# Optimization experiments

Hardware: AMD Instinct MI355X
Metric: run time of the kernel (lower is better)

## Reference

```python
import jax, jax.numpy as jnp
import numpy as np
from jax import lax

N = 8192
TARGET_COMPONENTS = 1.0
TARGET_CYCLES = 0.0
WEIGHT = 1.0
THRESH_SHIFT = 2.0


def setup_inputs() -> dict:
    key = jax.random.key(0)
    x = jax.random.normal(key, (N, N), dtype=jnp.float32)
    # symmetrize so directed DFS traversal == undirected connectivity,
    # then shift so adj > 0 is sparse (realistic learned graph structure)
    adj = (x + x.T) * 0.5 - THRESH_SHIFT
    return {"adj": adj}


def _count_components(adj):
    """Connected components via min-label propagation (parallel equivalent
    of the serial DFS in the torch module for a symmetric adjacency)."""
    n = adj.shape[0]
    pos = adj > 0  # [n, n] bool edge mask
    labels0 = jnp.arange(n, dtype=jnp.int32)

    def body(state):
        labels, _ = state
        # min label among neighbors (n = sentinel for non-edges)
        neigh_min = jnp.min(jnp.where(pos, labels[None, :], jnp.int32(n)), axis=1)
        new_labels = jnp.minimum(labels, neigh_min)
        return new_labels, jnp.any(new_labels != labels)

    labels, _ = lax.while_loop(lambda s: s[1], body,
                               (labels0, jnp.array(True)))
    # exactly one node per component keeps its own (minimal) index
    return jnp.sum((labels == labels0).astype(jnp.int32))


def reference(adj):
    n = adj.shape[0]
    n_comp = _count_components(adj).astype(jnp.float32)
    n_edges = (jnp.sum((adj > 0).astype(jnp.int32)) // 2).astype(jnp.float32)
    betti_1 = n_edges - jnp.float32(n) + n_comp           # Betti-1 estimate
    n_cycles = jnp.maximum(jnp.float32(0.0), betti_1)
    component_loss = (n_comp - TARGET_COMPONENTS) ** 2
    cycle_loss = (n_cycles - TARGET_CYCLES) ** 2
    return WEIGHT * (component_loss + cycle_loss)
```

## Files before the change

### kernel.cpp

```cpp
#include <hip/hip_runtime.h>


#define NN 8192
#define SCAN_LDS_CAP 2048

__global__ __launch_bounds__(64) void init_kernel(int* counters) {
    if (threadIdx.x < 2) counters[threadIdx.x] = 0;
}

__global__ __launch_bounds__(256) void scan_kernel(const float* __restrict__ adj,
                                                   int* __restrict__ counters,
                                                   unsigned int* __restrict__ ebuf,
                                                   int cap) {
    __shared__ int lds_n;
    __shared__ int lds_base;
    __shared__ unsigned int lds_e[SCAN_LDS_CAP];
    if (threadIdx.x == 0) lds_n = 0;
    __syncthreads();

    int b = blockIdx.x;
    int c1 = 0;
    #pragma unroll
    for (int half = 0; half < 2; ++half) {
        int r = half ? (NN - 1 - b) : b;
        const float4* rowp = (const float4*)(adj + (size_t)r * NN);
        int nf4 = (r + 4) >> 2;
        for (int g = threadIdx.x; g < nf4; g += 256) {
            float4 v = rowp[g];
            int j0 = g << 2;
            float vv[4] = {v.x, v.y, v.z, v.w};
            #pragma unroll
            for (int c = 0; c < 4; ++c) {
                int j = j0 + c;
                bool pos = vv[c] > 0.0f;
                if (pos && j < r) {
                    int k = atomicAdd(&lds_n, 1);
                    unsigned int e = ((unsigned)r << 13) | (unsigned)j;
                    if (k < SCAN_LDS_CAP) lds_e[k] = e;
                    else {
                        int gk = atomicAdd(counters, 1);
                        if (gk < cap) ebuf[gk] = e;
                    }
                }
                c1 += (pos && j == r) ? 1 : 0;
            }
        }
    }
    #pragma unroll
    for (int off = 32; off > 0; off >>= 1) c1 += __shfl_down(c1, off, 64);
    if ((threadIdx.x & 63) == 0 && c1) atomicAdd(counters + 1, c1);

    __syncthreads();
    int n = lds_n < SCAN_LDS_CAP ? lds_n : SCAN_LDS_CAP;
    if (threadIdx.x == 0) lds_base = atomicAdd(counters, n);
    __syncthreads();
    int base = lds_base;
    for (int k = threadIdx.x; k < n; k += 256) {
        int idx = base + k;
        if (idx < cap) ebuf[idx] = lds_e[k];
    }
}

__device__ __forceinline__ int find_lds(volatile int* par, int x) {
    int p = par[x];
    while (p != x) {
        int gp = par[p];
        if (gp == p) return p;
        par[x] = gp;
        x = gp;
        p = par[x];
    }
    return x;
}

__device__ __forceinline__ void unite_lds(int* par_raw, volatile int* par,
                                          int a, int b) {
    int ra = find_lds(par, a);
    int rb = find_lds(par, b);
    while (ra != rb) {
        int hi = ra > rb ? ra : rb;
        int lo = ra ^ rb ^ hi;
        int prev = atomicCAS(&par_raw[hi], hi, lo);
        if (prev == hi) return;
        ra = find_lds(par, prev);
        rb = find_lds(par, lo);
    }
}

__global__ __launch_bounds__(1024) void union_final_kernel(
        const unsigned int* __restrict__ ebuf,
        const int* __restrict__ counters,
        int cap, float* __restrict__ out) {
    __shared__ int par[NN];
    __shared__ int wsum[16];
    volatile int* vpar = par;
    int tid = threadIdx.x;
    for (int i = tid; i < NN; i += 1024) par[i] = i;
    __syncthreads();

    int total_lower = counters[0];
    int m = total_lower < cap ? total_lower : cap;

    const int CH = 16384;
    for (int base = 0; base < m; base += CH) {
        int hi = base + CH < m ? base + CH : m;
        for (int i = base + tid; i < hi; i += 1024) {
            unsigned int e = ebuf[i];
            unite_lds(par, vpar, (int)(e >> 13), (int)(e & (NN - 1)));
        }
        __syncthreads();
        for (int i = tid; i < NN; i += 1024) par[i] = find_lds(vpar, i);
        __syncthreads();
    }

    int cnt = 0;
    for (int i = tid; i < NN; i += 1024) cnt += (par[i] == i) ? 1 : 0;
    #pragma unroll
    for (int off = 32; off > 0; off >>= 1) cnt += __shfl_down(cnt, off, 64);
    if ((tid & 63) == 0) wsum[tid >> 6] = cnt;
    __syncthreads();
    if (tid == 0) {
        int roots = 0;
        #pragma unroll
        for (int w = 0; w < 16; ++w) roots += wsum[w];
        long long total = 2LL * (long long)total_lower + (long long)counters[1];
        long long n_edges_i = total >> 1;
        double n_comp = (double)roots;
        double comp_loss = (n_comp - 1.0) * (n_comp - 1.0);
        double betti = (double)n_edges_i - (double)NN + n_comp;
        double cyc = betti > 0.0 ? betti : 0.0;
        out[0] = (float)(comp_loss + cyc * cyc);
    }
}

extern "C" void kernel_launch(void* const* d_in, const int* in_sizes, int n_in,
                              void* d_out, int out_size, void* d_ws, size_t ws_size,
                              hipStream_t stream) {
    const float* adj = (const float*)d_in[0];
    int* ws = (int*)d_ws;
    int* counters = ws;
    unsigned int* ebuf = (unsigned int*)(ws + 2);
    long long cap_ll = (long long)(ws_size / 4) - 2;
    int cap = cap_ll > 0x7fffffff ? 0x7fffffff : (cap_ll < 0 ? 0 : (int)cap_ll);
    float* out = (float*)d_out;

    init_kernel<<<1, 64, 0, stream>>>(counters);
    scan_kernel<<<NN / 2, 256, 0, stream>>>(adj, counters, ebuf, cap);
    union_final_kernel<<<1, 1024, 0, stream>>>(ebuf, counters, cap, out);
}
```

Measured before the change: 436.9 us.

## Replace union-find with iterative min-label hooking and unroll scan row loads

The single-block component kernel drops the lock-free union-find and instead runs repeated passes over the edge list. Each pass hooks labels with atomicMin, then does one pointer-jumping step and loops until nothing changes. The scan kernel now issues four independent float4 loads per thread before processing them, to expose more memory-level parallelism. The label propagation may need many full passes over all ~78K edges in one block, which could cost more than the union-find did.

```diff
diff --git a/kernel.cpp b/kernel.cpp
--- a/kernel.cpp
+++ b/kernel.cpp
@@ -20,13 +20,14 @@
 
     int b = blockIdx.x;
     int c1 = 0;
+
     #pragma unroll
     for (int half = 0; half < 2; ++half) {
         int r = half ? (NN - 1 - b) : b;
         const float4* rowp = (const float4*)(adj + (size_t)r * NN);
         int nf4 = (r + 4) >> 2;
-        for (int g = threadIdx.x; g < nf4; g += 256) {
-            float4 v = rowp[g];
+
+        auto process = [&](float4 v, int g) {
             int j0 = g << 2;
             float vv[4] = {v.x, v.y, v.z, v.w};
             #pragma unroll
@@ -44,8 +45,22 @@
                 }
                 c1 += (pos && j == r) ? 1 : 0;
             }
+        };
+
+        int g = threadIdx.x;
+        for (; g + 768 < nf4; g += 1024) {
+            float4 v0 = rowp[g];
+            float4 v1 = rowp[g + 256];
+            float4 v2 = rowp[g + 512];
+            float4 v3 = rowp[g + 768];
+            process(v0, g);
+            process(v1, g + 256);
+            process(v2, g + 512);
+            process(v3, g + 768);
         }
+        for (; g < nf4; g += 256) process(rowp[g], g);
     }
+
     #pragma unroll
     for (int off = 32; off > 0; off >>= 1) c1 += __shfl_down(c1, off, 64);
     if ((threadIdx.x & 63) == 0 && c1) atomicAdd(counters + 1, c1);
@@ -61,60 +76,53 @@
     }
 }
 
-__device__ __forceinline__ int find_lds(volatile int* par, int x) {
-    int p = par[x];
-    while (p != x) {
-        int gp = par[p];
-        if (gp == p) return p;
-        par[x] = gp;
-        x = gp;
-        p = par[x];
-    }
-    return x;
-}
-
-__device__ __forceinline__ void unite_lds(int* par_raw, volatile int* par,
-                                          int a, int b) {
-    int ra = find_lds(par, a);
-    int rb = find_lds(par, b);
-    while (ra != rb) {
-        int hi = ra > rb ? ra : rb;
-        int lo = ra ^ rb ^ hi;
-        int prev = atomicCAS(&par_raw[hi], hi, lo);
-        if (prev == hi) return;
-        ra = find_lds(par, prev);
-        rb = find_lds(par, lo);
-    }
-}
-
-__global__ __launch_bounds__(1024) void union_final_kernel(
+__global__ __launch_bounds__(1024) void label_final_kernel(
         const unsigned int* __restrict__ ebuf,
         const int* __restrict__ counters,
         int cap, float* __restrict__ out) {
-    __shared__ int par[NN];
+    __shared__ int lab[NN];
+    __shared__ int changed;
     __shared__ int wsum[16];
-    volatile int* vpar = par;
     int tid = threadIdx.x;
-    for (int i = tid; i < NN; i += 1024) par[i] = i;
+    for (int i = tid; i < NN; i += 1024) lab[i] = i;
     __syncthreads();
 
     int total_lower = counters[0];
     int m = total_lower < cap ? total_lower : cap;
 
-    const int CH = 16384;
-    for (int base = 0; base < m; base += CH) {
-        int hi = base + CH < m ? base + CH : m;
-        for (int i = base + tid; i < hi; i += 1024) {
+    for (;;) {
+        if (tid == 0) changed = 0;
+        __syncthreads();
+
+        for (int i = tid; i < m; i += 1024) {
             unsigned int e = ebuf[i];
-            unite_lds(par, vpar, (int)(e >> 13), (int)(e & (NN - 1)));
+            int r = (int)(e >> 13);
+            int j = (int)(e & (NN - 1));
+            int lr = lab[r];
+            int lj = lab[j];
+            if (lj < lr) {
+                int old = atomicMin(&lab[r], lj);
+                if (lj < old) changed = 1;
+            } else if (lr < lj) {
+                int old = atomicMin(&lab[j], lr);
+                if (lr < old) changed = 1;
+            }
         }
         __syncthreads();
-        for (int i = tid; i < NN; i += 1024) par[i] = find_lds(vpar, i);
+
+        for (int i = tid; i < NN; i += 1024) {
+            int l = lab[i];
+            int ll = lab[l];
+            if (ll < l) { lab[i] = ll; changed = 1; }
+        }
+        __syncthreads();
+
+        if (changed == 0) break;
         __syncthreads();
     }
 
     int cnt = 0;
-    for (int i = tid; i < NN; i += 1024) cnt += (par[i] == i) ? 1 : 0;
+    for (int i = tid; i < NN; i += 1024) cnt += (lab[i] == i) ? 1 : 0;
     #pragma unroll
     for (int off = 32; off > 0; off >>= 1) cnt += __shfl_down(cnt, off, 64);
     if ((tid & 63) == 0) wsum[tid >> 6] = cnt;
@@ -146,5 +154,5 @@
 
     init_kernel<<<1, 64, 0, stream>>>(counters);
     scan_kernel<<<NN / 2, 256, 0, stream>>>(adj, counters, ebuf, cap);
-    union_final_kernel<<<1, 1024, 0, stream>>>(ebuf, counters, cap, out);
+    label_final_kernel<<<1, 1024, 0, stream>>>(ebuf, counters, cap, out);
 }
```

Result: faster. 414.5 us (-5.1%).
